# Kernel tuning notes

Hardware: AMD Instinct MI355X
Metric: run time of the kernel (lower is better)

## Reference

```python
import jax, jax.numpy as jnp
import numpy as np

HEADS = 16
PHI = (1.0 + np.sqrt(5.0)) / 2.0


def setup_inputs() -> dict:
    key = jax.random.key(0)
    k1, k2, k3, k4 = jax.random.split(key, 4)
    B, L, D = 2, 2048, 1024
    x = jax.random.normal(k1, (B, L, D), dtype=jnp.float32)
    # nn.Linear(dim, 3*dim, bias=False): store as [D, 3D] for x @ W
    w_qkv = jax.random.normal(k2, (D, 3 * D), dtype=jnp.float32) * (D ** -0.5)
    w_proj = jax.random.normal(k3, (D, D), dtype=jnp.float32) * (D ** -0.5)
    b_proj = jax.random.normal(k4, (D,), dtype=jnp.float32) * 0.01
    return {"x": x, "w_qkv": w_qkv, "w_proj": w_proj, "b_proj": b_proj}


def phi_bias(L):
    # pos[i] = (i * phi) mod 1 ; bias = log(exp(-|pos_i - pos_j|) + 1e-8)
    pos = (jnp.arange(L, dtype=jnp.float32) * PHI) % 1.0
    dist = jnp.abs(pos[:, None] - pos[None, :])  # [L, L]
    return jnp.log(jnp.exp(-dist) + 1e-8)


def reference(x, w_qkv, w_proj, b_proj):
    B, L, D = x.shape
    H = HEADS
    Dh = D // H
    scale = Dh ** -0.5
    qkv = (x @ w_qkv).reshape(B, L, 3, H, Dh)
    q = jnp.transpose(qkv[:, :, 0], (0, 2, 1, 3))  # [B, H, L, Dh]
    k = jnp.transpose(qkv[:, :, 1], (0, 2, 1, 3))
    v = jnp.transpose(qkv[:, :, 2], (0, 2, 1, 3))
    attn = jnp.einsum("bhid,bhjd->bhij", q, k) * scale  # [B, H, L, L]
    attn = attn + phi_bias(L)[None, None]  # additive phi-distance bias
    attn = jax.nn.softmax(attn, axis=-1)
    out = jnp.einsum("bhij,bhjd->bhid", attn, v)  # [B, H, L, Dh]
    out = jnp.transpose(out, (0, 2, 1, 3)).reshape(B, L, D)
    return out @ w_proj + b_proj
```

## Files before the change

### kernel.cpp

```cpp
#include <hip/hip_runtime.h>
#include <math.h>


typedef _Float16 f16;
typedef _Float16 f16x4 __attribute__((ext_vector_type(4)));
typedef _Float16 f16x8 __attribute__((ext_vector_type(8)));
typedef float f32x4 __attribute__((ext_vector_type(4)));

#define MFMA32(a, b, c) __builtin_amdgcn_mfma_f32_16x16x32_f16(a, b, c, 0, 0, 0)

static constexpr int Bsz = 2, Lseq = 2048, Dm = 1024, H = 16, Dh = 64;
static constexpr int Mtot = Bsz * Lseq;
static constexpr int NQKV = 3 * Dm;
static constexpr float PHI_F = 1.61803398874989484820f;
static constexpr float LOG2E = 1.44269504088896f;
static constexpr float QS = 0.125f * LOG2E;
static constexpr float CSTEP = 0.55417527999932633f;
static constexpr float C16 = 0.88854381999831757f;

__device__ __forceinline__ void load16_to_lds(const f16* g, f16* l) {
  __builtin_amdgcn_global_load_lds(
      (const __attribute__((address_space(1))) unsigned int*)g,
      (__attribute__((address_space(3))) unsigned int*)l, 16, 0, 0);
}

__global__ __launch_bounds__(256) void cast_f32_f16(const float* __restrict__ in,
                                                    f16* __restrict__ out, int n) {
  int i = (blockIdx.x * 256 + threadIdx.x) * 4;
  if (i < n) {
    float4 v = *reinterpret_cast<const float4*>(in + i);
    f16 t[4] = {(f16)v.x, (f16)v.y, (f16)v.z, (f16)v.w};
    *reinterpret_cast<uint2*>(out + i) = *reinterpret_cast<uint2*>(t);
  }
}

__global__ __launch_bounds__(256) void transpose_cast(const float* __restrict__ in,
                                                      f16* __restrict__ out,
                                                      int K, int N) {
  __shared__ float tile[32][33];
  int n0 = blockIdx.x * 32, k0 = blockIdx.y * 32;
  int tx = threadIdx.x & 31, ty = threadIdx.x >> 5;
#pragma unroll
  for (int r = 0; r < 32; r += 8)
    tile[ty + r][tx] = in[(size_t)(k0 + ty + r) * N + n0 + tx];
  __syncthreads();
#pragma unroll
  for (int r = 0; r < 32; r += 8)
    out[(size_t)(n0 + ty + r) * K + k0 + tx] = (f16)tile[tx][ty + r];
}

__global__ __launch_bounds__(256) void v_transpose(const f16* __restrict__ in,
                                                   f16* __restrict__ out) {
  __shared__ f16 td[64][68];
  int bh = blockIdx.y, l0 = blockIdx.x * 64;
  int tid = threadIdx.x;
  const f16* src = in + (size_t)bh * Lseq * Dh;
#pragma unroll
  for (int c = tid; c < 512; c += 256) {
    int row = c >> 3, col = (c & 7) * 8;
    uint4 v = *reinterpret_cast<const uint4*>(src + (size_t)(l0 + row) * Dh + col);
    f16 tmp[8];
    *reinterpret_cast<uint4*>(tmp) = v;
#pragma unroll
    for (int j = 0; j < 8; j++) td[col + j][row] = tmp[j];
  }
  __syncthreads();
  f16* dst = out + (size_t)bh * Dh * Lseq;
#pragma unroll
  for (int c = tid; c < 512; c += 256) {
    int d = c >> 3, co = c & 7;
    int jh = co >> 2, qd = co & 3;
    f16 tmp[8];
#pragma unroll
    for (int e = 0; e < 4; e++) tmp[e] = td[d][jh * 32 + qd * 4 + e];
#pragma unroll
    for (int e = 0; e < 4; e++) tmp[4 + e] = td[d][jh * 32 + 16 + qd * 4 + e];
    *reinterpret_cast<uint4*>(dst + (size_t)d * Lseq + l0 + co * 8) =
        *reinterpret_cast<uint4*>(tmp);
  }
}

template <int MODE>
__global__ __launch_bounds__(256) void gemm_f16(
    const f16* __restrict__ A, const f16* __restrict__ Bt,
    int M, int N, int K,
    f16* __restrict__ qb, f16* __restrict__ kb, f16* __restrict__ vl,
    float* __restrict__ out, const float* __restrict__ bias) {
  constexpr int BM = (MODE == 0) ? 128 : 64;
  constexpr int MI = BM / 32;
  constexpr int AI = BM / 32;
  __shared__ f16 As[BM * 64];
  __shared__ f16 Bs[128 * 64];

  int tid = threadIdx.x;
  int wave = tid >> 6, lane = tid & 63;
  int quad = lane >> 4, l16 = lane & 15;
  int wm = (wave >> 1) * (MI * 16), wn = (wave & 1) * 64;

  int lid = blockIdx.x;
  int xcd = lid & 7, t = lid >> 3;
  int m0, n0;
  if (MODE == 0) {
    int mg = xcd >> 1, ng = xcd & 1;
    m0 = (mg * 8 + t / 12) * 128;
    n0 = (ng * 12 + t % 12) * 128;
  } else {
    m0 = (xcd * 8 + (t >> 3)) * 64;
    n0 = (t & 7) * 128;
  }

  const int gu = (lane & 7) ^ (lane >> 3);
  const f16* gA[AI];
  f16* lA[AI];
#pragma unroll
  for (int i = 0; i < AI; i++) {
    int it = wave * AI + i;
    gA[i] = A + (size_t)(m0 + it * 8 + (lane >> 3)) * K + gu * 8;
    lA[i] = As + it * 512;
  }
  const f16* gB[4];
  f16* lB[4];
#pragma unroll
  for (int i = 0; i < 4; i++) {
    int it = wave * 4 + i;
    gB[i] = Bt + (size_t)(n0 + it * 8 + (lane >> 3)) * K + gu * 8;
    lB[i] = Bs + it * 512;
  }

  f32x4 acc[MI][4] = {};

  for (int k0 = 0; k0 < K; k0 += 64) {
#pragma unroll
    for (int i = 0; i < AI; i++) load16_to_lds(gA[i] + k0, lA[i]);
#pragma unroll
    for (int i = 0; i < 4; i++) load16_to_lds(gB[i] + k0, lB[i]);
    __syncthreads();
#pragma unroll
    for (int s = 0; s < 2; s++) {
      f16x8 a[MI], b[4];
#pragma unroll
      for (int i = 0; i < MI; i++) {
        int row = wm + i * 16 + l16;
        a[i] = *reinterpret_cast<const f16x8*>(
            As + row * 64 + (((s * 4 + quad) ^ (l16 & 7)) * 8));
      }
#pragma unroll
      for (int j = 0; j < 4; j++) {
        int row = wn + j * 16 + l16;
        b[j] = *reinterpret_cast<const f16x8*>(
            Bs + row * 64 + (((s * 4 + quad) ^ (l16 & 7)) * 8));
      }
#pragma unroll
      for (int i = 0; i < MI; i++)
#pragma unroll
        for (int j = 0; j < 4; j++)
          acc[i][j] = MFMA32(a[i], b[j], acc[i][j]);
    }
    __syncthreads();
  }

#pragma unroll
  for (int i = 0; i < MI; i++) {
#pragma unroll
    for (int j = 0; j < 4; j++) {
      int n = n0 + wn + j * 16 + l16;
#pragma unroll
      for (int r = 0; r < 4; r++) {
        int m = m0 + wm + i * 16 + quad * 4 + r;
        if (MODE == 0) {
          int ty = n >> 10;
          int df = n & 1023;
          int h = df >> 6, dh = df & 63;
          int b = m >> 11, l = m & 2047;
          size_t idx = (((size_t)(b * H + h)) * Lseq + l) * Dh + dh;
          if (ty == 0)
            qb[idx] = (f16)(acc[i][j][r] * QS);
          else if (ty == 1)
            kb[idx] = (f16)acc[i][j][r];
          else
            vl[idx] = (f16)acc[i][j][r];
        } else {
          out[(size_t)m * N + n] = acc[i][j][r] + bias[n];
        }
      }
    }
  }
}

__global__ __launch_bounds__(512, 8) void attn_kernel(
    const f16* __restrict__ qb,
    const f16* __restrict__ kb,
    const f16* __restrict__ vb,
    f16* __restrict__ ctx) {
  __shared__ __align__(16) unsigned char smem[16640];
  f16* Ks = (f16*)smem;
  f16* Vs = (f16*)(smem + 8192);

  int bh = blockIdx.y;
  int q0 = blockIdx.x * 64;
  int tid = threadIdx.x, wave = tid >> 6, lane = tid & 63;
  int quad = lane >> 4, l16 = lane & 15;
  int jhalf = wave >> 2, qq = wave & 3;

  int q = q0 + qq * 16 + l16;
  const f16* Qrow = qb + ((size_t)bh * Lseq + q) * Dh;
  f16x8 qfrag0 = *reinterpret_cast<const f16x8*>(Qrow + quad * 8);
  f16x8 qfrag1 = *reinterpret_cast<const f16x8*>(Qrow + 32 + quad * 8);
  float pq = fmodf((float)q * PHI_F, 1.0f);

  float pk0[4];
#pragma unroll
  for (int r = 0; r < 4; r++) {
    int j = jhalf * 32 + quad * 4 + r;
    pk0[r] = fmodf((float)j * PHI_F, 1.0f);
  }

  const int gu = (lane & 7) ^ (lane >> 3);
  int g8 = wave * 8 + (lane >> 3);
  const f16* gK = kb + (size_t)bh * Lseq * Dh + (size_t)g8 * Dh + gu * 8;
  const f16* gV = vb + (size_t)bh * Dh * Lseq + (size_t)g8 * Lseq + gu * 8;
  f16* lK = Ks + wave * 512;
  f16* lV = Vs + wave * 512;

  const f16 one = (f16)1.0f;
  const f16x8 ones8 = {one, one, one, one, one, one, one, one};

  f32x4 acc_o[4] = {};
  f32x4 acc_l = {};

  const f16* kfp0 = Ks + (jhalf * 32 + l16) * 64 + ((quad ^ (l16 & 7)) * 8);
  const f16* kfp1 = Ks + (jhalf * 32 + l16) * 64 + (((4 + quad) ^ (l16 & 7)) * 8);
  const f16* vfp = Vs + l16 * 64 + (((jhalf * 4 + quad) ^ (l16 & 7)) * 8);

#pragma unroll 1
  for (int j0 = 0; j0 < Lseq; j0 += 64) {
    __syncthreads();
    load16_to_lds(gK + (size_t)j0 * Dh, lK);
    load16_to_lds(gV + j0, lV);
    __syncthreads();

    f32x4 accs[2];
    float pk1[4];
#pragma unroll
    for (int r = 0; r < 4; r++) {
      accs[0][r] = -LOG2E * fabsf(pq - pk0[r]);
      pk1[r] = __builtin_amdgcn_fractf(pk0[r] + C16);
    }
#pragma unroll
    for (int r = 0; r < 4; r++) {
      accs[1][r] = -LOG2E * fabsf(pq - pk1[r]);
      pk0[r] = __builtin_amdgcn_fractf(pk0[r] + CSTEP);
    }

    __builtin_amdgcn_s_setprio(1);
    {
      f16x8 kf00 = *reinterpret_cast<const f16x8*>(kfp0);
      f16x8 kf01 = *reinterpret_cast<const f16x8*>(kfp1);
      f16x8 kf10 = *reinterpret_cast<const f16x8*>(kfp0 + 16 * 64);
      f16x8 kf11 = *reinterpret_cast<const f16x8*>(kfp1 + 16 * 64);
      accs[0] = MFMA32(kf00, qfrag0, accs[0]);
      accs[0] = MFMA32(kf01, qfrag1, accs[0]);
      accs[1] = MFMA32(kf10, qfrag0, accs[1]);
      accs[1] = MFMA32(kf11, qfrag1, accs[1]);
    }
    __builtin_amdgcn_s_setprio(0);

    f16x8 pf8;
#pragma unroll
    for (int jb = 0; jb < 2; jb++) {
      float p[4];
#pragma unroll
      for (int r = 0; r < 4; r++) p[r] = __builtin_amdgcn_exp2f(accs[jb][r]);
      auto lo = __builtin_amdgcn_cvt_pkrtz(p[0], p[1]);
      auto hi = __builtin_amdgcn_cvt_pkrtz(p[2], p[3]);
      pf8[jb * 4 + 0] = lo[0];
      pf8[jb * 4 + 1] = lo[1];
      pf8[jb * 4 + 2] = hi[0];
      pf8[jb * 4 + 3] = hi[1];
    }
    acc_l = MFMA32(ones8, pf8, acc_l);

    __builtin_amdgcn_s_setprio(1);
#pragma unroll
    for (int dblk = 0; dblk < 4; dblk++) {
      f16x8 va = *reinterpret_cast<const f16x8*>(vfp + dblk * 16 * 64);
      acc_o[dblk] = MFMA32(va, pf8, acc_o[dblk]);
    }
    __builtin_amdgcn_s_setprio(0);
  }

  __syncthreads();
  float* Oex = (float*)smem;
  float* Lex = (float*)(smem + 16384);
  if (jhalf == 1) {
#pragma unroll
    for (int dblk = 0; dblk < 4; dblk++)
#pragma unroll
      for (int r = 0; r < 4; r++)
        Oex[((qq * 4 + dblk) * 16 + quad * 4 + r) * 16 + l16] = acc_o[dblk][r];
    if (quad == 0) Lex[qq * 16 + l16] = acc_l[0];
  }
  __syncthreads();
  if (jhalf == 0) {
    int b = bh >> 4, h = bh & 15;
    float ltot = acc_l[0] + Lex[qq * 16 + l16];
    float inv = 1.0f / ltot;
    f16* crow = ctx + (size_t)(b * Lseq + q) * Dm + h * 64;
#pragma unroll
    for (int dblk = 0; dblk < 4; dblk++) {
      f16x4 o;
#pragma unroll
      for (int r = 0; r < 4; r++) {
        float full = acc_o[dblk][r] +
            Oex[((qq * 4 + dblk) * 16 + quad * 4 + r) * 16 + l16];
        o[r] = (f16)(full * inv);
      }
      *reinterpret_cast<uint2*>(crow + dblk * 16 + quad * 4) =
          *reinterpret_cast<uint2*>(&o);
    }
  }
}

extern "C" void kernel_launch(void* const* d_in, const int* in_sizes, int n_in,
                              void* d_out, int out_size, void* d_ws, size_t ws_size,
                              hipStream_t stream) {
  const float* x      = (const float*)d_in[0];
  const float* w_qkv  = (const float*)d_in[1];
  const float* w_proj = (const float*)d_in[2];
  const float* b_proj = (const float*)d_in[3];
  float* out = (float*)d_out;

  f16* xb    = (f16*)d_ws;
  f16* wqkvT = xb + (size_t)Mtot * Dm;
  f16* wpT   = wqkvT + (size_t)NQKV * Dm;
  f16* qb    = wpT + (size_t)Dm * Dm;
  f16* kb    = qb + (size_t)Bsz * H * Lseq * Dh;
  f16* vb    = kb + (size_t)Bsz * H * Lseq * Dh;
  f16* ctx   = vb + (size_t)Bsz * H * Lseq * Dh;
  f16* vl    = ctx;

  cast_f32_f16<<<(Mtot * Dm) / (256 * 4), 256, 0, stream>>>(x, xb, Mtot * Dm);
  transpose_cast<<<dim3(NQKV / 32, Dm / 32), 256, 0, stream>>>(w_qkv, wqkvT, Dm, NQKV);
  transpose_cast<<<dim3(Dm / 32, Dm / 32), 256, 0, stream>>>(w_proj, wpT, Dm, Dm);

  gemm_f16<0><<<768, 256, 0, stream>>>(
      xb, wqkvT, Mtot, NQKV, Dm, qb, kb, vl, nullptr, nullptr);

  v_transpose<<<dim3(Lseq / 64, Bsz * H), 256, 0, stream>>>(vl, vb);

  attn_kernel<<<dim3(Lseq / 64, Bsz * H), 512, 0, stream>>>(qb, kb, vb, ctx);

  gemm_f16<1><<<512, 256, 0, stream>>>(
      ctx, wpT, Mtot, Dm, Dm, nullptr, nullptr, nullptr, out, b_proj);
}
```

Baseline: 206.6 us.

## Load K/V fragments directly from global memory with XCD-aware block mapping

The attention kernel drops the per-tile LDS staging and its two barriers per iteration, and instead has each wave read K and V MFMA fragments straight from global memory (relying on L2/cache reuse). V is re-laid out by the transpose kernel into 64x64 tiles so the fragment reads are contiguous. Blocks are shrunk to 256 threads covering 32 queries each and remapped so heads are grouped per XCD, aiming for L2 locality of K/V. The trade-off is more global/L2 traffic and latency exposure per wave without the shared-memory reuse across waves.

After: 446.0 us. +115.9%, slower.

```diff
diff --git a/kernel.cpp b/kernel.cpp
--- a/kernel.cpp
+++ b/kernel.cpp
@@ -65,7 +65,7 @@
     for (int j = 0; j < 8; j++) td[col + j][row] = tmp[j];
   }
   __syncthreads();
-  f16* dst = out + (size_t)bh * Dh * Lseq;
+  f16* dst = out + (size_t)bh * Dh * Lseq + (size_t)(l0 >> 6) * 4096;
 #pragma unroll
   for (int c = tid; c < 512; c += 256) {
     int d = c >> 3, co = c & 7;
@@ -75,7 +75,7 @@
     for (int e = 0; e < 4; e++) tmp[e] = td[d][jh * 32 + qd * 4 + e];
 #pragma unroll
     for (int e = 0; e < 4; e++) tmp[4 + e] = td[d][jh * 32 + 16 + qd * 4 + e];
-    *reinterpret_cast<uint4*>(dst + (size_t)d * Lseq + l0 + co * 8) =
+    *reinterpret_cast<uint4*>(dst + d * 64 + co * 8) =
         *reinterpret_cast<uint4*>(tmp);
   }
 }
@@ -187,22 +187,23 @@
   }
 }
 
-__global__ __launch_bounds__(512, 8) void attn_kernel(
+__global__ __launch_bounds__(256, 6) void attn_kernel(
     const f16* __restrict__ qb,
     const f16* __restrict__ kb,
     const f16* __restrict__ vb,
     f16* __restrict__ ctx) {
-  __shared__ __align__(16) unsigned char smem[16640];
-  f16* Ks = (f16*)smem;
-  f16* Vs = (f16*)(smem + 8192);
-
-  int bh = blockIdx.y;
-  int q0 = blockIdx.x * 64;
+  __shared__ __align__(16) unsigned char smem[8448];
+
+  int id = blockIdx.x;
+  int xcd = id & 7, t = id >> 3;
+  int bh = ((t >> 6) << 3) + xcd;
+  int q0 = (t & 63) * 32;
+
   int tid = threadIdx.x, wave = tid >> 6, lane = tid & 63;
   int quad = lane >> 4, l16 = lane & 15;
-  int jhalf = wave >> 2, qq = wave & 3;
-
-  int q = q0 + qq * 16 + l16;
+  int strip = wave >> 1, jhalf = wave & 1;
+
+  int q = q0 + strip * 16 + l16;
   const f16* Qrow = qb + ((size_t)bh * Lseq + q) * Dh;
   f16x8 qfrag0 = *reinterpret_cast<const f16x8*>(Qrow + quad * 8);
   f16x8 qfrag1 = *reinterpret_cast<const f16x8*>(Qrow + 32 + quad * 8);
@@ -215,12 +216,11 @@
     pk0[r] = fmodf((float)j * PHI_F, 1.0f);
   }
 
-  const int gu = (lane & 7) ^ (lane >> 3);
-  int g8 = wave * 8 + (lane >> 3);
-  const f16* gK = kb + (size_t)bh * Lseq * Dh + (size_t)g8 * Dh + gu * 8;
-  const f16* gV = vb + (size_t)bh * Dh * Lseq + (size_t)g8 * Lseq + gu * 8;
-  f16* lK = Ks + wave * 512;
-  f16* lV = Vs + wave * 512;
+  const f16* pK = kb + (size_t)bh * Lseq * Dh + (size_t)(jhalf * 32 + l16) * 64 +
+                  quad * 8;
+  const f16* pVa = vb + (size_t)bh * Dh * Lseq + (size_t)l16 * 64 +
+                   jhalf * 32 + quad * 8;
+  const f16* pVb = pVa + 2048;
 
   const f16 one = (f16)1.0f;
   const f16x8 ones8 = {one, one, one, one, one, one, one, one};
@@ -228,82 +228,79 @@
   f32x4 acc_o[4] = {};
   f32x4 acc_l = {};
 
-  const f16* kfp0 = Ks + (jhalf * 32 + l16) * 64 + ((quad ^ (l16 & 7)) * 8);
-  const f16* kfp1 = Ks + (jhalf * 32 + l16) * 64 + (((4 + quad) ^ (l16 & 7)) * 8);
-  const f16* vfp = Vs + l16 * 64 + (((jhalf * 4 + quad) ^ (l16 & 7)) * 8);
-
 #pragma unroll 1
-  for (int j0 = 0; j0 < Lseq; j0 += 64) {
-    __syncthreads();
-    load16_to_lds(gK + (size_t)j0 * Dh, lK);
-    load16_to_lds(gV + j0, lV);
-    __syncthreads();
-
-    f32x4 accs[2];
+  for (int it = 0; it < 32; ++it) {
+    f16x8 kf00 = *reinterpret_cast<const f16x8*>(pK);
+    f16x8 kf01 = *reinterpret_cast<const f16x8*>(pK + 32);
+    f16x8 kf10 = *reinterpret_cast<const f16x8*>(pK + 1024);
+    f16x8 kf11 = *reinterpret_cast<const f16x8*>(pK + 1056);
+
+    f32x4 accs0, accs1;
     float pk1[4];
 #pragma unroll
     for (int r = 0; r < 4; r++) {
-      accs[0][r] = -LOG2E * fabsf(pq - pk0[r]);
+      accs0[r] = -LOG2E * fabsf(pq - pk0[r]);
       pk1[r] = __builtin_amdgcn_fractf(pk0[r] + C16);
     }
 #pragma unroll
     for (int r = 0; r < 4; r++) {
-      accs[1][r] = -LOG2E * fabsf(pq - pk1[r]);
+      accs1[r] = -LOG2E * fabsf(pq - pk1[r]);
       pk0[r] = __builtin_amdgcn_fractf(pk0[r] + CSTEP);
     }
 
-    __builtin_amdgcn_s_setprio(1);
+    accs0 = MFMA32(kf00, qfrag0, accs0);
+    accs0 = MFMA32(kf01, qfrag1, accs0);
+    accs1 = MFMA32(kf10, qfrag0, accs1);
+    accs1 = MFMA32(kf11, qfrag1, accs1);
+
+    f16x8 pf8;
     {
-      f16x8 kf00 = *reinterpret_cast<const f16x8*>(kfp0);
-      f16x8 kf01 = *reinterpret_cast<const f16x8*>(kfp1);
-      f16x8 kf10 = *reinterpret_cast<const f16x8*>(kfp0 + 16 * 64);
-      f16x8 kf11 = *reinterpret_cast<const f16x8*>(kfp1 + 16 * 64);
-      accs[0] = MFMA32(kf00, qfrag0, accs[0]);
-      accs[0] = MFMA32(kf01, qfrag1, accs[0]);
-      accs[1] = MFMA32(kf10, qfrag0, accs[1]);
-      accs[1] = MFMA32(kf11, qfrag1, accs[1]);
-    }
-    __builtin_amdgcn_s_setprio(0);
-
-    f16x8 pf8;
-#pragma unroll
-    for (int jb = 0; jb < 2; jb++) {
-      float p[4];
-#pragma unroll
-      for (int r = 0; r < 4; r++) p[r] = __builtin_amdgcn_exp2f(accs[jb][r]);
-      auto lo = __builtin_amdgcn_cvt_pkrtz(p[0], p[1]);
-      auto hi = __builtin_amdgcn_cvt_pkrtz(p[2], p[3]);
-      pf8[jb * 4 + 0] = lo[0];
-      pf8[jb * 4 + 1] = lo[1];
-      pf8[jb * 4 + 2] = hi[0];
-      pf8[jb * 4 + 3] = hi[1];
+      float p0 = __builtin_amdgcn_exp2f(accs0[0]);
+      float p1 = __builtin_amdgcn_exp2f(accs0[1]);
+      float p2 = __builtin_amdgcn_exp2f(accs0[2]);
+      float p3 = __builtin_amdgcn_exp2f(accs0[3]);
+      auto lo = __builtin_amdgcn_cvt_pkrtz(p0, p1);
+      auto hi = __builtin_amdgcn_cvt_pkrtz(p2, p3);
+      pf8[0] = lo[0]; pf8[1] = lo[1]; pf8[2] = hi[0]; pf8[3] = hi[1];
+      p0 = __builtin_amdgcn_exp2f(accs1[0]);
+      p1 = __builtin_amdgcn_exp2f(accs1[1]);
+      p2 = __builtin_amdgcn_exp2f(accs1[2]);
+      p3 = __builtin_amdgcn_exp2f(accs1[3]);
+      lo = __builtin_amdgcn_cvt_pkrtz(p0, p1);
+      hi = __builtin_amdgcn_cvt_pkrtz(p2, p3);
+      pf8[4] = lo[0]; pf8[5] = lo[1]; pf8[6] = hi[0]; pf8[7] = hi[1];
     }
     acc_l = MFMA32(ones8, pf8, acc_l);
 
-    __builtin_amdgcn_s_setprio(1);
-#pragma unroll
-    for (int dblk = 0; dblk < 4; dblk++) {
-      f16x8 va = *reinterpret_cast<const f16x8*>(vfp + dblk * 16 * 64);
-      acc_o[dblk] = MFMA32(va, pf8, acc_o[dblk]);
-    }
-    __builtin_amdgcn_s_setprio(0);
-  }
-
-  __syncthreads();
+    f16x8 va0 = *reinterpret_cast<const f16x8*>(pVa);
+    f16x8 va1 = *reinterpret_cast<const f16x8*>(pVa + 1024);
+    f16x8 va2 = *reinterpret_cast<const f16x8*>(pVb);
+    f16x8 va3 = *reinterpret_cast<const f16x8*>(pVb + 1024);
+    acc_o[0] = MFMA32(va0, pf8, acc_o[0]);
+    acc_o[1] = MFMA32(va1, pf8, acc_o[1]);
+    acc_o[2] = MFMA32(va2, pf8, acc_o[2]);
+    acc_o[3] = MFMA32(va3, pf8, acc_o[3]);
+
+    pK += 4096;
+    pVa += 4096;
+    pVb += 4096;
+  }
+
   float* Oex = (float*)smem;
-  float* Lex = (float*)(smem + 16384);
+  float* Lex = (float*)(smem + 8192);
   if (jhalf == 1) {
 #pragma unroll
     for (int dblk = 0; dblk < 4; dblk++)
 #pragma unroll
       for (int r = 0; r < 4; r++)
-        Oex[((qq * 4 + dblk) * 16 + quad * 4 + r) * 16 + l16] = acc_o[dblk][r];
-    if (quad == 0) Lex[qq * 16 + l16] = acc_l[0];
+        Oex[((strip * 4 + dblk) * 16 + quad * 4 + r) * 16 + l16] =
+            acc_o[dblk][r];
+    if (quad == 0) Lex[strip * 16 + l16] = acc_l[0];
   }
   __syncthreads();
   if (jhalf == 0) {
     int b = bh >> 4, h = bh & 15;
-    float ltot = acc_l[0] + Lex[qq * 16 + l16];
+    float ltot = acc_l[0] + Lex[strip * 16 + l16];
     float inv = 1.0f / ltot;
     f16* crow = ctx + (size_t)(b * Lseq + q) * Dm + h * 64;
 #pragma unroll
@@ -312,7 +309,7 @@
 #pragma unroll
       for (int r = 0; r < 4; r++) {
         float full = acc_o[dblk][r] +
-            Oex[((qq * 4 + dblk) * 16 + quad * 4 + r) * 16 + l16];
+            Oex[((strip * 4 + dblk) * 16 + quad * 4 + r) * 16 + l16];
         o[r] = (f16)(full * inv);
       }
       *reinterpret_cast<uint2*>(crow + dblk * 16 + quad * 4) =
@@ -348,7 +345,7 @@
 
   v_transpose<<<dim3(Lseq / 64, Bsz * H), 256, 0, stream>>>(vl, vb);
 
-  attn_kernel<<<dim3(Lseq / 64, Bsz * H), 512, 0, stream>>>(qb, kb, vb, ctx);
+  attn_kernel<<<2048, 256, 0, stream>>>(qb, kb, vb, ctx);
 
   gemm_f16<1><<<512, 256, 0, stream>>>(
       ctx, wpT, Mtot, Dm, Dm, nullptr, nullptr, nullptr, out, b_proj);
```
